# Kernel optimization log

Measured on AMD Instinct MI355X. Metric: run time of the kernel, lower is better.

The kernel has to match this reference:

```python
import jax, jax.numpy as jnp
import numpy as np

N_NODES = 50000
N_EDGES = 800000
D = 128        # in_channels == out_channels
EDGE_DIM = 32
EPS = 0.0      # GINEConv default eps


def setup_inputs() -> dict:
    key = jax.random.key(0)
    ks = jax.random.split(key, 12)
    s = lambda d: 1.0 / np.sqrt(d)
    inp = {
        "x": jax.random.normal(ks[0], (N_NODES, D), jnp.float32),
        "edge_index": jax.random.randint(ks[1], (2, N_EDGES), 0, N_NODES, jnp.int64),
        "edge_attr": jax.random.normal(ks[2], (N_EDGES, EDGE_DIM), jnp.float32),
        "importance": jax.random.uniform(ks[3], (N_NODES, 1), jnp.float32),
        # GINEConv edge lin: Linear(edge_dim, in_channels)
        "We": jax.random.uniform(ks[4], (EDGE_DIM, D), jnp.float32, -s(EDGE_DIM), s(EDGE_DIM)),
        "be": jax.random.uniform(ks[5], (D,), jnp.float32, -s(EDGE_DIM), s(EDGE_DIM)),
        # GINEConv nn: Linear(in_channels, out_channels)
        "Wc": jax.random.uniform(ks[6], (D, D), jnp.float32, -s(D), s(D)),
        "bc": jax.random.uniform(ks[7], (D,), jnp.float32, -s(D), s(D)),
        # importance_gate: Linear(out_channels + 1, out_channels)
        "Wg": jax.random.uniform(ks[8], (D + 1, D), jnp.float32, -s(D + 1), s(D + 1)),
        "bg": jax.random.uniform(ks[9], (D,), jnp.float32, -s(D + 1), s(D + 1)),
        # importance_propagation: Linear(out_channels, 1)
        "Wp": jax.random.uniform(ks[10], (D, 1), jnp.float32, -s(D), s(D)),
        "bp": jax.random.uniform(ks[11], (1,), jnp.float32, -s(D), s(D)),
    }
    return inp


def reference(x, edge_index, edge_attr, importance, We, be, Wc, bc, Wg, bg, Wp, bp):
    src, dst = edge_index[0], edge_index[1]
    # GINEConv: messages = relu(x_j + lin(edge_attr)), aggregated by sum at dst
    e = edge_attr @ We + be                      # [E, D]
    msg = jax.nn.relu(x[src] + e)                # [E, D] gather + fused add/relu
    agg = jax.ops.segment_sum(msg, dst, num_segments=N_NODES)  # [N, D] scatter-add
    conv_out = ((1.0 + EPS) * x + agg) @ Wc + bc  # [N, D]
    # importance gating + residual
    gate_in = jnp.concatenate([conv_out, importance], axis=-1)  # [N, D+1]
    gate = jax.nn.sigmoid(gate_in @ Wg + bg)
    out = gate * conv_out + (1.0 - gate) * x
    propagated_importance = out @ Wp + bp        # [N, 1]
    return (out, propagated_importance)
```

## Files before the change

### kernel.cpp

```cpp
#include <hip/hip_runtime.h>

#define NN 50000
#define NE 800000
#define DD 128
#define ED 32
#define NB 196

typedef short bf16x8 __attribute__((ext_vector_type(8)));
typedef float f32x4  __attribute__((ext_vector_type(4)));

__device__ __forceinline__ float4 ld4(const float* p) {
    return *reinterpret_cast<const float4*>(p);
}
__device__ __forceinline__ short f2bf(float f) {
    unsigned u = __float_as_uint(f);
    u += 0x7fffu + ((u >> 16) & 1u);
    return (short)(u >> 16);
}
__device__ __forceinline__ float bf2f(short h) {
    return __uint_as_float(((unsigned)(unsigned short)h) << 16);
}
__device__ __forceinline__ int sniff64(const int* ei) {
    return ((ei[1] | ei[3] | ei[5] | ei[7]) == 0) ? 1 : 0;
}

__global__ __launch_bounds__(256)
void k_hist(const int* __restrict__ ei, int* __restrict__ counts) {
    const int is64 = sniff64(ei);
    for (int e = blockIdx.x * blockDim.x + threadIdx.x; e < NE;
         e += gridDim.x * blockDim.x) {
        const int dst = ei[(long)(NE + e) << is64];
        atomicAdd(&counts[dst], 1);
    }
}

__global__ __launch_bounds__(256)
void k_bsum(const int* __restrict__ counts, int* __restrict__ bsum) {
    const int i = blockIdx.x * 256 + threadIdx.x;
    int c = (i < NN) ? counts[i] : 0;
#pragma unroll
    for (int off = 32; off; off >>= 1) c += __shfl_xor(c, off, 64);
    __shared__ int ws4[4];
    if ((threadIdx.x & 63) == 0) ws4[threadIdx.x >> 6] = c;
    __syncthreads();
    if (threadIdx.x == 0) bsum[blockIdx.x] = ws4[0] + ws4[1] + ws4[2] + ws4[3];
}

__global__ __launch_bounds__(256)
void k_scanb(const int* __restrict__ bsum, int* __restrict__ bexcl) {
    const int tid = threadIdx.x, lane = tid & 63, w = tid >> 6;
    const int v = (tid < NB) ? bsum[tid] : 0;
    int s = v;
#pragma unroll
    for (int off = 1; off < 64; off <<= 1) {
        const int t = __shfl_up(s, off, 64);
        if (lane >= off) s += t;
    }
    __shared__ int wsum[4], wexcl[4];
    if (lane == 63) wsum[w] = s;
    __syncthreads();
    if (tid == 0) {
        int r = 0;
#pragma unroll
        for (int k = 0; k < 4; ++k) { wexcl[k] = r; r += wsum[k]; }
    }
    __syncthreads();
    if (tid < NB) bexcl[tid] = wexcl[w] + s - v;
}

__global__ __launch_bounds__(256)
void k_rowptr(const int* __restrict__ counts, const int* __restrict__ bexcl,
              int* __restrict__ rowptr, int* __restrict__ cursor) {
    const int tid = threadIdx.x, lane = tid & 63, w = tid >> 6;
    const int i = blockIdx.x * 256 + tid;
    const int c = (i < NN) ? counts[i] : 0;
    int s = c;
#pragma unroll
    for (int off = 1; off < 64; off <<= 1) {
        const int t = __shfl_up(s, off, 64);
        if (lane >= off) s += t;
    }
    __shared__ int wsum[4], wexcl[4];
    if (lane == 63) wsum[w] = s;
    __syncthreads();
    if (tid == 0) {
        int r = 0;
#pragma unroll
        for (int k = 0; k < 4; ++k) { wexcl[k] = r; r += wsum[k]; }
    }
    __syncthreads();
    const int excl = bexcl[blockIdx.x] + wexcl[w] + s - c;
    if (i < NN) { rowptr[i] = excl; cursor[i] = excl; }
    if (blockIdx.x == 0 && tid == 0) rowptr[NN] = NE;
}

__global__ __launch_bounds__(256)
void k_scatter(const int* __restrict__ ei, int* __restrict__ cursor,
               int2* __restrict__ sdat) {
    const int is64 = sniff64(ei);
    for (int e = blockIdx.x * blockDim.x + threadIdx.x; e < NE;
         e += gridDim.x * blockDim.x) {
        const int src = ei[(long)e << is64];
        const int dst = ei[(long)(NE + e) << is64];
        const int pos = atomicAdd(&cursor[dst], 1);
        sdat[pos] = make_int2(src, e);
    }
}

__global__ __launch_bounds__(256, 2)
void k_agg(const float* __restrict__ x, const float* __restrict__ ea,
           const float* __restrict__ We, const float* __restrict__ be,
           const int* __restrict__ rowptr, const int2* __restrict__ sdat,
           float* __restrict__ pre)
{
    const int lane = threadIdx.x & 63;
    const int wid  = (blockIdx.x << 2) | (threadIdx.x >> 6);
    const int ncol = lane & 15;
    const int krow = (lane >> 4) << 3;
    const int grp  = lane >> 4;

    bf16x8 Bf[8];
    float beb[8];
#pragma unroll
    for (int b = 0; b < 8; ++b) {
#pragma unroll
        for (int i = 0; i < 8; ++i)
            Bf[b][i] = f2bf(We[(krow + i) * DD + b * 16 + ncol]);
        beb[b] = be[b * 16 + ncol];
    }

    const int nA = wid, nB = wid + NN / 2;
    int cbA = rowptr[nA]; const int endA = rowptr[nA + 1];
    int cbB = rowptr[nB]; const int endB = rowptr[nB + 1];
    float aA0 = 0.f, aA1 = 0.f, aB0 = 0.f, aB1 = 0.f;

    while (cbA < endA || cbB < endB) {
        const bool dA = cbA < endA, dB = cbB < endB;
        const int cntA = dA ? min(16, endA - cbA) : 0;
        const int cntB = dB ? min(16, endB - cbB) : 0;
        int2 dvA = make_int2(0, 0), dvB = make_int2(0, 0);
        if (dA && lane < cntA) dvA = sdat[cbA + lane];
        if (dB && lane < cntB) dvB = sdat[cbB + lane];

        bf16x8 AfA = {}, AfB = {};
        f32x4 CA[8], CB[8];
        float mA[4], mB[4];

        if (dA) {
            const int eidx = __shfl(dvA.y, ncol, 64);
            const float* ear = ea + (size_t)eidx * ED + krow;
            const float4 r0 = ld4(ear), r1 = ld4(ear + 4);
            AfA[0] = f2bf(r0.x); AfA[1] = f2bf(r0.y);
            AfA[2] = f2bf(r0.z); AfA[3] = f2bf(r0.w);
            AfA[4] = f2bf(r1.x); AfA[5] = f2bf(r1.y);
            AfA[6] = f2bf(r1.z); AfA[7] = f2bf(r1.w);
            const float* xr[4];
#pragma unroll
            for (int r = 0; r < 4; ++r) {
                const int m = (grp << 2) + r;
                xr[r] = x + (size_t)__shfl(dvA.x, m, 64) * DD + ncol;
                mA[r] = (m < cntA) ? 1.0f : 0.0f;
            }
#pragma unroll
            for (int b = 0; b < 8; ++b) {
                f32x4 c;
                c[0] = xr[0][b * 16]; c[1] = xr[1][b * 16];
                c[2] = xr[2][b * 16]; c[3] = xr[3][b * 16];
                CA[b] = c;
            }
        }
        if (dB) {
            const int eidx = __shfl(dvB.y, ncol, 64);
            const float* ear = ea + (size_t)eidx * ED + krow;
            const float4 r0 = ld4(ear), r1 = ld4(ear + 4);
            AfB[0] = f2bf(r0.x); AfB[1] = f2bf(r0.y);
            AfB[2] = f2bf(r0.z); AfB[3] = f2bf(r0.w);
            AfB[4] = f2bf(r1.x); AfB[5] = f2bf(r1.y);
            AfB[6] = f2bf(r1.z); AfB[7] = f2bf(r1.w);
            const float* xr[4];
#pragma unroll
            for (int r = 0; r < 4; ++r) {
                const int m = (grp << 2) + r;
                xr[r] = x + (size_t)__shfl(dvB.x, m, 64) * DD + ncol;
                mB[r] = (m < cntB) ? 1.0f : 0.0f;
            }
#pragma unroll
            for (int b = 0; b < 8; ++b) {
                f32x4 c;
                c[0] = xr[0][b * 16]; c[1] = xr[1][b * 16];
                c[2] = xr[2][b * 16]; c[3] = xr[3][b * 16];
                CB[b] = c;
            }
        }

        if (dA) {
#pragma unroll
            for (int b = 0; b < 8; ++b)
                CA[b] = __builtin_amdgcn_mfma_f32_16x16x32_bf16(AfA, Bf[b], CA[b], 0, 0, 0);
        }
        if (dB) {
#pragma unroll
            for (int b = 0; b < 8; ++b)
                CB[b] = __builtin_amdgcn_mfma_f32_16x16x32_bf16(AfB, Bf[b], CB[b], 0, 0, 0);
        }

        if (dA) {
            float red[8];
#pragma unroll
            for (int b = 0; b < 8; ++b) {
                float t = fmaxf(CA[b][0] + beb[b], 0.f) * mA[0]
                        + fmaxf(CA[b][1] + beb[b], 0.f) * mA[1]
                        + fmaxf(CA[b][2] + beb[b], 0.f) * mA[2]
                        + fmaxf(CA[b][3] + beb[b], 0.f) * mA[3];
                t += __shfl_xor(t, 16, 64);
                t += __shfl_xor(t, 32, 64);
                red[b] = t;
            }
            float v0 = red[0], v1 = red[4];
            v0 = (grp == 1) ? red[1] : v0;
            v0 = (grp == 2) ? red[2] : v0;
            v0 = (grp == 3) ? red[3] : v0;
            v1 = (grp == 1) ? red[5] : v1;
            v1 = (grp == 2) ? red[6] : v1;
            v1 = (grp == 3) ? red[7] : v1;
            aA0 += v0; aA1 += v1;
            cbA += 16;
        }
        if (dB) {
            float red[8];
#pragma unroll
            for (int b = 0; b < 8; ++b) {
                float t = fmaxf(CB[b][0] + beb[b], 0.f) * mB[0]
                        + fmaxf(CB[b][1] + beb[b], 0.f) * mB[1]
                        + fmaxf(CB[b][2] + beb[b], 0.f) * mB[2]
                        + fmaxf(CB[b][3] + beb[b], 0.f) * mB[3];
                t += __shfl_xor(t, 16, 64);
                t += __shfl_xor(t, 32, 64);
                red[b] = t;
            }
            float v0 = red[0], v1 = red[4];
            v0 = (grp == 1) ? red[1] : v0;
            v0 = (grp == 2) ? red[2] : v0;
            v0 = (grp == 3) ? red[3] : v0;
            v1 = (grp == 1) ? red[5] : v1;
            v1 = (grp == 2) ? red[6] : v1;
            v1 = (grp == 3) ? red[7] : v1;
            aB0 += v0; aB1 += v1;
            cbB += 16;
        }
    }

    {
        const size_t oA = (size_t)nA * DD;
        pre[oA + lane]      = aA0 + x[oA + lane];
        pre[oA + 64 + lane] = aA1 + x[oA + 64 + lane];
        const size_t oB = (size_t)nB * DD;
        pre[oB + lane]      = aB0 + x[oB + lane];
        pre[oB + 64 + lane] = aB1 + x[oB + 64 + lane];
    }
}

__global__ __launch_bounds__(256)
void k_conv(const float* __restrict__ pre, const float* __restrict__ Wc,
            const float* __restrict__ bc, float* __restrict__ conv)
{
    __shared__ short sBh[2048 * 8];
    __shared__ short sBl[2048 * 8];
    for (int idx = threadIdx.x; idx < 2048; idx += 256) {
        const int kk = idx >> 9;
        const int b  = (idx >> 6) & 7;
        const int l  = idx & 63;
        const int row0 = kk * 32 + ((l >> 4) << 3);
        const int col  = b * 16 + (l & 15);
        bf16x8 h8, l8;
#pragma unroll
        for (int j = 0; j < 8; ++j) {
            const float v = Wc[(row0 + j) * DD + col];
            const short h = f2bf(v);
            h8[j] = h;
            l8[j] = f2bf(v - bf2f(h));
        }
        *reinterpret_cast<bf16x8*>(&sBh[idx * 8]) = h8;
        *reinterpret_cast<bf16x8*>(&sBl[idx * 8]) = l8;
    }
    __syncthreads();

    const int lane = threadIdx.x & 63;
    const int ncol = lane & 15;
    const int krow = (lane >> 4) << 3;
    const int grp  = lane >> 4;
    const int wid  = (blockIdx.x << 2) | (threadIdx.x >> 6);
    if (wid >= NN / 16) return;

    float bcb[8];
#pragma unroll
    for (int b = 0; b < 8; ++b) bcb[b] = bc[b * 16 + ncol];

    const int m0 = wid * 16;
    const float* arow = pre + (size_t)(m0 + ncol) * DD + krow;

    f32x4 C[8];
#pragma unroll
    for (int b = 0; b < 8; ++b) {
        f32x4 c = { bcb[b], bcb[b], bcb[b], bcb[b] };
        C[b] = c;
    }

#pragma unroll
    for (int kk = 0; kk < 4; ++kk) {
        const float4 a0 = ld4(arow + kk * 32);
        const float4 a1 = ld4(arow + kk * 32 + 4);
        const float av[8] = { a0.x, a0.y, a0.z, a0.w, a1.x, a1.y, a1.z, a1.w };
        bf16x8 Ah, Al;
#pragma unroll
        for (int j = 0; j < 8; ++j) {
            const short h = f2bf(av[j]);
            Ah[j] = h;
            Al[j] = f2bf(av[j] - bf2f(h));
        }
#pragma unroll
        for (int b = 0; b < 8; ++b) {
            const bf16x8 Bh = *reinterpret_cast<const bf16x8*>(&sBh[((kk * 8 + b) * 64 + lane) * 8]);
            const bf16x8 Bl = *reinterpret_cast<const bf16x8*>(&sBl[((kk * 8 + b) * 64 + lane) * 8]);
            C[b] = __builtin_amdgcn_mfma_f32_16x16x32_bf16(Ah, Bh, C[b], 0, 0, 0);
            C[b] = __builtin_amdgcn_mfma_f32_16x16x32_bf16(Al, Bh, C[b], 0, 0, 0);
            C[b] = __builtin_amdgcn_mfma_f32_16x16x32_bf16(Ah, Bl, C[b], 0, 0, 0);
        }
    }

#pragma unroll
    for (int r = 0; r < 4; ++r) {
        float* crow = conv + (size_t)(m0 + (grp << 2) + r) * DD + ncol;
#pragma unroll
        for (int b = 0; b < 8; ++b) crow[b * 16] = C[b][r];
    }
}

__global__ __launch_bounds__(256)
void k_gate(const float* __restrict__ x, const float* conv,
            const float* __restrict__ imp, const float* __restrict__ Wg,
            const float* __restrict__ bg, const float* __restrict__ Wp,
            const float* __restrict__ bp, float* outp, float* __restrict__ prop)
{
    __shared__ short sBh[2048 * 8];
    __shared__ short sBl[2048 * 8];
    for (int idx = threadIdx.x; idx < 2048; idx += 256) {
        const int kk = idx >> 9;
        const int b  = (idx >> 6) & 7;
        const int l  = idx & 63;
        const int row0 = kk * 32 + ((l >> 4) << 3);
        const int col  = b * 16 + (l & 15);
        bf16x8 h8, l8;
#pragma unroll
        for (int j = 0; j < 8; ++j) {
            const float v = Wg[(row0 + j) * DD + col];
            const short h = f2bf(v);
            h8[j] = h;
            l8[j] = f2bf(v - bf2f(h));
        }
        *reinterpret_cast<bf16x8*>(&sBh[idx * 8]) = h8;
        *reinterpret_cast<bf16x8*>(&sBl[idx * 8]) = l8;
    }
    __syncthreads();

    const int lane = threadIdx.x & 63;
    const int ncol = lane & 15;
    const int krow = (lane >> 4) << 3;
    const int grp  = lane >> 4;
    const int wid  = (blockIdx.x << 2) | (threadIdx.x >> 6);
    if (wid >= NN / 16) return;

    float bgb[8], wgi[8], wp8[8];
#pragma unroll
    for (int b = 0; b < 8; ++b) {
        bgb[b] = bg[b * 16 + ncol];
        wgi[b] = Wg[DD * DD + b * 16 + ncol];
        wp8[b] = Wp[b * 16 + ncol];
    }
    const float bps = bp[0];

    const int m0 = wid * 16;

    float cvD[8][4], xvD[8][4], im[4];
#pragma unroll
    for (int r = 0; r < 4; ++r) {
        const int m = m0 + (grp << 2) + r;
        const float* cr = conv + (size_t)m * DD + ncol;
        const float* xr = x    + (size_t)m * DD + ncol;
        im[r] = imp[m];
#pragma unroll
        for (int b = 0; b < 8; ++b) { cvD[b][r] = cr[b * 16]; xvD[b][r] = xr[b * 16]; }
    }

    f32x4 C[8];
#pragma unroll
    for (int b = 0; b < 8; ++b) {
        f32x4 c = { bgb[b], bgb[b], bgb[b], bgb[b] };
        C[b] = c;
    }

    const float* arow = conv + (size_t)(m0 + ncol) * DD + krow;
#pragma unroll
    for (int kk = 0; kk < 4; ++kk) {
        const float4 a0 = ld4(arow + kk * 32);
        const float4 a1 = ld4(arow + kk * 32 + 4);
        const float av[8] = { a0.x, a0.y, a0.z, a0.w, a1.x, a1.y, a1.z, a1.w };
        bf16x8 Ah, Al;
#pragma unroll
        for (int j = 0; j < 8; ++j) {
            const short h = f2bf(av[j]);
            Ah[j] = h;
            Al[j] = f2bf(av[j] - bf2f(h));
        }
#pragma unroll
        for (int b = 0; b < 8; ++b) {
            const bf16x8 Bh = *reinterpret_cast<const bf16x8*>(&sBh[((kk * 8 + b) * 64 + lane) * 8]);
            const bf16x8 Bl = *reinterpret_cast<const bf16x8*>(&sBl[((kk * 8 + b) * 64 + lane) * 8]);
            C[b] = __builtin_amdgcn_mfma_f32_16x16x32_bf16(Ah, Bh, C[b], 0, 0, 0);
            C[b] = __builtin_amdgcn_mfma_f32_16x16x32_bf16(Al, Bh, C[b], 0, 0, 0);
            C[b] = __builtin_amdgcn_mfma_f32_16x16x32_bf16(Ah, Bl, C[b], 0, 0, 0);
        }
    }

    float s[4] = { 0.f, 0.f, 0.f, 0.f };
#pragma unroll
    for (int r = 0; r < 4; ++r) {
        float* orow = outp + (size_t)(m0 + (grp << 2) + r) * DD + ncol;
#pragma unroll
        for (int b = 0; b < 8; ++b) {
            const float a = C[b][r] + im[r] * wgi[b];
            const float g = 1.0f / (1.0f + expf(-a));
            const float o = fmaf(g, cvD[b][r] - xvD[b][r], xvD[b][r]);
            orow[b * 16] = o;
            s[r] += o * wp8[b];
        }
    }
#pragma unroll
    for (int off = 1; off < 16; off <<= 1) {
        s[0] += __shfl_xor(s[0], off, 64);
        s[1] += __shfl_xor(s[1], off, 64);
        s[2] += __shfl_xor(s[2], off, 64);
        s[3] += __shfl_xor(s[3], off, 64);
    }
    if (ncol < 4) {
        const float v = (ncol == 0) ? s[0] : (ncol == 1) ? s[1] : (ncol == 2) ? s[2] : s[3];
        prop[m0 + (grp << 2) + ncol] = v + bps;
    }
}

extern "C" void kernel_launch(void* const* d_in, const int* in_sizes, int n_in,
                              void* d_out, int out_size, void* d_ws, size_t ws_size,
                              hipStream_t stream) {
    const float* x   = (const float*)d_in[0];
    const int*   ei  = (const int*)d_in[1];
    const float* ea  = (const float*)d_in[2];
    const float* imp = (const float*)d_in[3];
    const float* We  = (const float*)d_in[4];
    const float* be  = (const float*)d_in[5];
    const float* Wc  = (const float*)d_in[6];
    const float* bc  = (const float*)d_in[7];
    const float* Wg  = (const float*)d_in[8];
    const float* bg  = (const float*)d_in[9];
    const float* Wp  = (const float*)d_in[10];
    const float* bp  = (const float*)d_in[11];

    float* out  = (float*)d_out;
    float* prop = out + (size_t)NN * DD;

    float* pre    = (float*)d_ws;
    int*   bsum   = (int*)d_ws;
    int*   bexcl  = (int*)((char*)d_ws + 4096);
    int*   counts = (int*)((char*)d_ws + 25600000);
    int*   rowptr = (int*)((char*)d_ws + 25800000);
    int*   cursor = (int*)((char*)d_ws + 26000064);
    int2*  sdat   = (int2*)((char*)d_ws + 26200192);

    hipMemsetAsync(counts, 0, NN * sizeof(int), stream);
    hipLaunchKernelGGL(k_hist,    dim3(2048), dim3(256), 0, stream, ei, counts);
    hipLaunchKernelGGL(k_bsum,    dim3(NB),   dim3(256), 0, stream, counts, bsum);
    hipLaunchKernelGGL(k_scanb,   dim3(1),    dim3(256), 0, stream, bsum, bexcl);
    hipLaunchKernelGGL(k_rowptr,  dim3(NB),   dim3(256), 0, stream, counts, bexcl, rowptr, cursor);
    hipLaunchKernelGGL(k_scatter, dim3(2048), dim3(256), 0, stream, ei, cursor, sdat);
    hipLaunchKernelGGL(k_agg,     dim3(6250), dim3(256), 0, stream,
                       x, ea, We, be, rowptr, sdat, pre);
    hipLaunchKernelGGL(k_conv,    dim3(782),  dim3(256), 0, stream, pre, Wc, bc, out);
    hipLaunchKernelGGL(k_gate,    dim3(782),  dim3(256), 0, stream,
                       x, out, imp, Wg, bg, Wp, bp, out, prop);
}
```

Baseline: 231.4 us.

## Switch aggregation to edge-parallel chunks with segmented reduce and atomics

The per-node aggregation, where each wave walked one destination's edge list, is replaced by an edge-parallel kernel. Each wave processes fixed chunks of 16 sorted edges, finds destination segments with a ballot, reduces per segment, and atomically adds the sums into an agg buffer stored in the output. The self term x is now added inside the conv kernel, rowptr is dropped, and a per-edge destination array is written during scatter. This removes load imbalance and partial-chunk waste from uneven degrees, but adds float atomics, an extra memset of the agg buffer, and another edge-sized array to write and read.

New measurement: 236.4 us. 2.1% more time.

```diff
diff --git a/kernel.cpp b/kernel.cpp
--- a/kernel.cpp
+++ b/kernel.cpp
@@ -5,6 +5,7 @@
 #define DD 128
 #define ED 32
 #define NB 196
+#define NCH (NE / 16)
 
 typedef short bf16x8 __attribute__((ext_vector_type(8)));
 typedef float f32x4  __attribute__((ext_vector_type(4)));
@@ -70,7 +71,7 @@
 
 __global__ __launch_bounds__(256)
 void k_rowptr(const int* __restrict__ counts, const int* __restrict__ bexcl,
-              int* __restrict__ rowptr, int* __restrict__ cursor) {
+              int* __restrict__ cursor) {
     const int tid = threadIdx.x, lane = tid & 63, w = tid >> 6;
     const int i = blockIdx.x * 256 + tid;
     const int c = (i < NN) ? counts[i] : 0;
@@ -89,14 +90,12 @@
         for (int k = 0; k < 4; ++k) { wexcl[k] = r; r += wsum[k]; }
     }
     __syncthreads();
-    const int excl = bexcl[blockIdx.x] + wexcl[w] + s - c;
-    if (i < NN) { rowptr[i] = excl; cursor[i] = excl; }
-    if (blockIdx.x == 0 && tid == 0) rowptr[NN] = NE;
+    if (i < NN) cursor[i] = bexcl[blockIdx.x] + wexcl[w] + s - c;
 }
 
 __global__ __launch_bounds__(256)
 void k_scatter(const int* __restrict__ ei, int* __restrict__ cursor,
-               int2* __restrict__ sdat) {
+               int2* __restrict__ sdat, int* __restrict__ edst) {
     const int is64 = sniff64(ei);
     for (int e = blockIdx.x * blockDim.x + threadIdx.x; e < NE;
          e += gridDim.x * blockDim.x) {
@@ -104,20 +103,22 @@
         const int dst = ei[(long)(NE + e) << is64];
         const int pos = atomicAdd(&cursor[dst], 1);
         sdat[pos] = make_int2(src, e);
-    }
-}
-
-__global__ __launch_bounds__(256, 2)
-void k_agg(const float* __restrict__ x, const float* __restrict__ ea,
-           const float* __restrict__ We, const float* __restrict__ be,
-           const int* __restrict__ rowptr, const int2* __restrict__ sdat,
-           float* __restrict__ pre)
+        edst[pos] = dst;
+    }
+}
+
+__global__ __launch_bounds__(256, 4)
+void k_aggE(const float* __restrict__ x, const float* __restrict__ ea,
+            const float* __restrict__ We, const float* __restrict__ be,
+            const int2* __restrict__ sdat, const int* __restrict__ edst,
+            float* __restrict__ agg)
 {
     const int lane = threadIdx.x & 63;
-    const int wid  = (blockIdx.x << 2) | (threadIdx.x >> 6);
     const int ncol = lane & 15;
     const int krow = (lane >> 4) << 3;
     const int grp  = lane >> 4;
+    const int wid  = (blockIdx.x << 2) | (threadIdx.x >> 6);
+    const int nw   = gridDim.x << 2;
 
     bf16x8 Bf[8];
     float beb[8];
@@ -129,92 +130,76 @@
         beb[b] = be[b * 16 + ncol];
     }
 
-    const int nA = wid, nB = wid + NN / 2;
-    int cbA = rowptr[nA]; const int endA = rowptr[nA + 1];
-    int cbB = rowptr[nB]; const int endB = rowptr[nB + 1];
-    float aA0 = 0.f, aA1 = 0.f, aB0 = 0.f, aB1 = 0.f;
-
-    while (cbA < endA || cbB < endB) {
-        const bool dA = cbA < endA, dB = cbB < endB;
-        const int cntA = dA ? min(16, endA - cbA) : 0;
-        const int cntB = dB ? min(16, endB - cbB) : 0;
-        int2 dvA = make_int2(0, 0), dvB = make_int2(0, 0);
-        if (dA && lane < cntA) dvA = sdat[cbA + lane];
-        if (dB && lane < cntB) dvB = sdat[cbB + lane];
-
-        bf16x8 AfA = {}, AfB = {};
-        f32x4 CA[8], CB[8];
-        float mA[4], mB[4];
-
-        if (dA) {
-            const int eidx = __shfl(dvA.y, ncol, 64);
-            const float* ear = ea + (size_t)eidx * ED + krow;
-            const float4 r0 = ld4(ear), r1 = ld4(ear + 4);
-            AfA[0] = f2bf(r0.x); AfA[1] = f2bf(r0.y);
-            AfA[2] = f2bf(r0.z); AfA[3] = f2bf(r0.w);
-            AfA[4] = f2bf(r1.x); AfA[5] = f2bf(r1.y);
-            AfA[6] = f2bf(r1.z); AfA[7] = f2bf(r1.w);
-            const float* xr[4];
-#pragma unroll
-            for (int r = 0; r < 4; ++r) {
-                const int m = (grp << 2) + r;
-                xr[r] = x + (size_t)__shfl(dvA.x, m, 64) * DD + ncol;
-                mA[r] = (m < cntA) ? 1.0f : 0.0f;
-            }
+    if (wid >= NCH) return;
+
+    int2 dv   = sdat[wid * 16 + ncol];
+    int  dstv = edst[wid * 16 + ncol];
+
+    for (int c = wid; c < NCH; c += nw) {
+        const int cn = min(c + nw, NCH - 1);
+        const int2 dvn   = sdat[cn * 16 + ncol];
+        const int  dstvn = edst[cn * 16 + ncol];
+
+        const float* ear = ea + (size_t)dv.y * ED + krow;
+        const float4 r0 = ld4(ear), r1 = ld4(ear + 4);
+
+        const float* xr[4];
+#pragma unroll
+        for (int r = 0; r < 4; ++r)
+            xr[r] = x + (size_t)__shfl(dv.x, (grp << 2) + r, 64) * DD + ncol;
+        f32x4 C[8];
+#pragma unroll
+        for (int b = 0; b < 8; ++b) {
+            f32x4 cc;
+            cc[0] = xr[0][b * 16]; cc[1] = xr[1][b * 16];
+            cc[2] = xr[2][b * 16]; cc[3] = xr[3][b * 16];
+            C[b] = cc;
+        }
+
+        bf16x8 Af;
+        Af[0] = f2bf(r0.x); Af[1] = f2bf(r0.y);
+        Af[2] = f2bf(r0.z); Af[3] = f2bf(r0.w);
+        Af[4] = f2bf(r1.x); Af[5] = f2bf(r1.y);
+        Af[6] = f2bf(r1.z); Af[7] = f2bf(r1.w);
+
+#pragma unroll
+        for (int b = 0; b < 8; ++b)
+            C[b] = __builtin_amdgcn_mfma_f32_16x16x32_bf16(Af, Bf[b], C[b], 0, 0, 0);
+
+        float t[8][4];
+#pragma unroll
+        for (int b = 0; b < 8; ++b)
+#pragma unroll
+            for (int r = 0; r < 4; ++r)
+                t[b][r] = fmaxf(C[b][r] + beb[b], 0.0f);
+
+        const int prv = __shfl(dstv, (lane == 0) ? 0 : lane - 1, 64);
+        const bool flag = (lane < 16) && ((ncol == 0) || (dstv != prv));
+        const unsigned B16 = (unsigned)__ballot(flag) & 0xFFFFu;
+
+        int sid[4];
+#pragma unroll
+        for (int r = 0; r < 4; ++r) {
+            const int m = (grp << 2) + r;
+            sid[r] = __popc(B16 & ((2u << m) - 1)) - 1;
+        }
+
+        unsigned rem = B16;
+        int s = 0;
+        while (rem) {
+            const int ms = __ffs((int)rem) - 1;
+            rem &= rem - 1;
+            const int d = __shfl(dstv, ms, 64);
+            float red[8];
 #pragma unroll
             for (int b = 0; b < 8; ++b) {
-                f32x4 c;
-                c[0] = xr[0][b * 16]; c[1] = xr[1][b * 16];
-                c[2] = xr[2][b * 16]; c[3] = xr[3][b * 16];
-                CA[b] = c;
-            }
-        }
-        if (dB) {
-            const int eidx = __shfl(dvB.y, ncol, 64);
-            const float* ear = ea + (size_t)eidx * ED + krow;
-            const float4 r0 = ld4(ear), r1 = ld4(ear + 4);
-            AfB[0] = f2bf(r0.x); AfB[1] = f2bf(r0.y);
-            AfB[2] = f2bf(r0.z); AfB[3] = f2bf(r0.w);
-            AfB[4] = f2bf(r1.x); AfB[5] = f2bf(r1.y);
-            AfB[6] = f2bf(r1.z); AfB[7] = f2bf(r1.w);
-            const float* xr[4];
-#pragma unroll
-            for (int r = 0; r < 4; ++r) {
-                const int m = (grp << 2) + r;
-                xr[r] = x + (size_t)__shfl(dvB.x, m, 64) * DD + ncol;
-                mB[r] = (m < cntB) ? 1.0f : 0.0f;
-            }
-#pragma unroll
-            for (int b = 0; b < 8; ++b) {
-                f32x4 c;
-                c[0] = xr[0][b * 16]; c[1] = xr[1][b * 16];
-                c[2] = xr[2][b * 16]; c[3] = xr[3][b * 16];
-                CB[b] = c;
-            }
-        }
-
-        if (dA) {
-#pragma unroll
-            for (int b = 0; b < 8; ++b)
-                CA[b] = __builtin_amdgcn_mfma_f32_16x16x32_bf16(AfA, Bf[b], CA[b], 0, 0, 0);
-        }
-        if (dB) {
-#pragma unroll
-            for (int b = 0; b < 8; ++b)
-                CB[b] = __builtin_amdgcn_mfma_f32_16x16x32_bf16(AfB, Bf[b], CB[b], 0, 0, 0);
-        }
-
-        if (dA) {
-            float red[8];
-#pragma unroll
-            for (int b = 0; b < 8; ++b) {
-                float t = fmaxf(CA[b][0] + beb[b], 0.f) * mA[0]
-                        + fmaxf(CA[b][1] + beb[b], 0.f) * mA[1]
-                        + fmaxf(CA[b][2] + beb[b], 0.f) * mA[2]
-                        + fmaxf(CA[b][3] + beb[b], 0.f) * mA[3];
-                t += __shfl_xor(t, 16, 64);
-                t += __shfl_xor(t, 32, 64);
-                red[b] = t;
+                float v = ((sid[0] == s) ? t[b][0] : 0.0f)
+                        + ((sid[1] == s) ? t[b][1] : 0.0f)
+                        + ((sid[2] == s) ? t[b][2] : 0.0f)
+                        + ((sid[3] == s) ? t[b][3] : 0.0f);
+                v += __shfl_xor(v, 16, 64);
+                v += __shfl_xor(v, 32, 64);
+                red[b] = v;
             }
             float v0 = red[0], v1 = red[4];
             v0 = (grp == 1) ? red[1] : v0;
@@ -223,46 +208,20 @@
             v1 = (grp == 1) ? red[5] : v1;
             v1 = (grp == 2) ? red[6] : v1;
             v1 = (grp == 3) ? red[7] : v1;
-            aA0 += v0; aA1 += v1;
-            cbA += 16;
-        }
-        if (dB) {
-            float red[8];
-#pragma unroll
-            for (int b = 0; b < 8; ++b) {
-                float t = fmaxf(CB[b][0] + beb[b], 0.f) * mB[0]
-                        + fmaxf(CB[b][1] + beb[b], 0.f) * mB[1]
-                        + fmaxf(CB[b][2] + beb[b], 0.f) * mB[2]
-                        + fmaxf(CB[b][3] + beb[b], 0.f) * mB[3];
-                t += __shfl_xor(t, 16, 64);
-                t += __shfl_xor(t, 32, 64);
-                red[b] = t;
-            }
-            float v0 = red[0], v1 = red[4];
-            v0 = (grp == 1) ? red[1] : v0;
-            v0 = (grp == 2) ? red[2] : v0;
-            v0 = (grp == 3) ? red[3] : v0;
-            v1 = (grp == 1) ? red[5] : v1;
-            v1 = (grp == 2) ? red[6] : v1;
-            v1 = (grp == 3) ? red[7] : v1;
-            aB0 += v0; aB1 += v1;
-            cbB += 16;
-        }
-    }
-
-    {
-        const size_t oA = (size_t)nA * DD;
-        pre[oA + lane]      = aA0 + x[oA + lane];
-        pre[oA + 64 + lane] = aA1 + x[oA + 64 + lane];
-        const size_t oB = (size_t)nB * DD;
-        pre[oB + lane]      = aB0 + x[oB + lane];
-        pre[oB + 64 + lane] = aB1 + x[oB + 64 + lane];
-    }
-}
-
-__global__ __launch_bounds__(256)
-void k_conv(const float* __restrict__ pre, const float* __restrict__ Wc,
-            const float* __restrict__ bc, float* __restrict__ conv)
+            float* ar = agg + (size_t)d * DD;
+            unsafeAtomicAdd(ar + lane, v0);
+            unsafeAtomicAdd(ar + 64 + lane, v1);
+            ++s;
+        }
+
+        dv = dvn; dstv = dstvn;
+    }
+}
+
+__global__ __launch_bounds__(256)
+void k_conv(const float* __restrict__ x, const float* agg,
+            const float* __restrict__ Wc, const float* __restrict__ bc,
+            float* conv)
 {
     __shared__ short sBh[2048 * 8];
     __shared__ short sBl[2048 * 8];
@@ -297,7 +256,8 @@
     for (int b = 0; b < 8; ++b) bcb[b] = bc[b * 16 + ncol];
 
     const int m0 = wid * 16;
-    const float* arow = pre + (size_t)(m0 + ncol) * DD + krow;
+    const float* xrow = x   + (size_t)(m0 + ncol) * DD + krow;
+    const float* grow = agg + (size_t)(m0 + ncol) * DD + krow;
 
     f32x4 C[8];
 #pragma unroll
@@ -308,9 +268,10 @@
 
 #pragma unroll
     for (int kk = 0; kk < 4; ++kk) {
-        const float4 a0 = ld4(arow + kk * 32);
-        const float4 a1 = ld4(arow + kk * 32 + 4);
-        const float av[8] = { a0.x, a0.y, a0.z, a0.w, a1.x, a1.y, a1.z, a1.w };
+        const float4 x0 = ld4(xrow + kk * 32), x1 = ld4(xrow + kk * 32 + 4);
+        const float4 g0 = ld4(grow + kk * 32), g1 = ld4(grow + kk * 32 + 4);
+        const float av[8] = { x0.x + g0.x, x0.y + g0.y, x0.z + g0.z, x0.w + g0.w,
+                              x1.x + g1.x, x1.y + g1.y, x1.z + g1.z, x1.w + g1.w };
         bf16x8 Ah, Al;
 #pragma unroll
         for (int j = 0; j < 8; ++j) {
@@ -466,24 +427,25 @@
 
     float* out  = (float*)d_out;
     float* prop = out + (size_t)NN * DD;
-
-    float* pre    = (float*)d_ws;
-    int*   bsum   = (int*)d_ws;
-    int*   bexcl  = (int*)((char*)d_ws + 4096);
-    int*   counts = (int*)((char*)d_ws + 25600000);
-    int*   rowptr = (int*)((char*)d_ws + 25800000);
-    int*   cursor = (int*)((char*)d_ws + 26000064);
-    int2*  sdat   = (int2*)((char*)d_ws + 26200192);
+    float* agg  = out;
+
+    int*  counts = (int*)d_ws;
+    int*  cursor = (int*)((char*)d_ws + 204800);
+    int*  bsum   = (int*)((char*)d_ws + 409600);
+    int*  bexcl  = (int*)((char*)d_ws + 413696);
+    int2* sdat   = (int2*)((char*)d_ws + 1048576);
+    int*  edst   = (int*)((char*)d_ws + 7448576);
 
     hipMemsetAsync(counts, 0, NN * sizeof(int), stream);
+    hipMemsetAsync(agg, 0, (size_t)NN * DD * sizeof(float), stream);
     hipLaunchKernelGGL(k_hist,    dim3(2048), dim3(256), 0, stream, ei, counts);
     hipLaunchKernelGGL(k_bsum,    dim3(NB),   dim3(256), 0, stream, counts, bsum);
     hipLaunchKernelGGL(k_scanb,   dim3(1),    dim3(256), 0, stream, bsum, bexcl);
-    hipLaunchKernelGGL(k_rowptr,  dim3(NB),   dim3(256), 0, stream, counts, bexcl, rowptr, cursor);
-    hipLaunchKernelGGL(k_scatter, dim3(2048), dim3(256), 0, stream, ei, cursor, sdat);
-    hipLaunchKernelGGL(k_agg,     dim3(6250), dim3(256), 0, stream,
-                       x, ea, We, be, rowptr, sdat, pre);
-    hipLaunchKernelGGL(k_conv,    dim3(782),  dim3(256), 0, stream, pre, Wc, bc, out);
+    hipLaunchKernelGGL(k_rowptr,  dim3(NB),   dim3(256), 0, stream, counts, bexcl, cursor);
+    hipLaunchKernelGGL(k_scatter, dim3(2048), dim3(256), 0, stream, ei, cursor, sdat, edst);
+    hipLaunchKernelGGL(k_aggE,    dim3(2048), dim3(256), 0, stream,
+                       x, ea, We, be, sdat, edst, agg);
+    hipLaunchKernelGGL(k_conv,    dim3(782),  dim3(256), 0, stream, x, agg, Wc, bc, out);
     hipLaunchKernelGGL(k_gate,    dim3(782),  dim3(256), 0, stream,
                        x, out, imp, Wg, bg, Wp, bp, out, prop);
 }
```
